# Optimization experiments

Hardware: AMD Instinct MI355X
Metric: run time of the kernel (lower is better)

Reference implementation:

```python
import jax, jax.numpy as jnp
import numpy as np

VOCAB = 50000
WORD_DIM = 300
PAT_LEN = 6
DOC_LEN = 32768


def setup_inputs() -> dict:
    key = jax.random.key(0)
    k1, k2, k3, k4 = jax.random.split(key, 4)
    doc = jax.random.randint(k1, (DOC_LEN,), 0, VOCAB, dtype=jnp.int64)
    embeddings = jax.random.normal(k2, (VOCAB, WORD_DIM), dtype=jnp.float32)
    w = jax.random.normal(k3, (PAT_LEN, PAT_LEN, WORD_DIM), dtype=jnp.float32)
    # original code normalizes each w[i, j] to unit norm at init
    w = w / jnp.linalg.norm(w, axis=-1, keepdims=True)
    b = jax.random.normal(k4, (PAT_LEN, PAT_LEN), dtype=jnp.float32)
    return {"doc": doc, "embeddings": embeddings, "w": w, "b": b}


def reference(doc, embeddings, w, b):
    p = w.shape[0]
    # Only the superdiagonal (i, i+1) of the transition matrix is nonzero.
    idx = jnp.arange(p - 1)
    w_sd = w[idx, idx + 1]          # [p-1, d]
    b_sd = b[idx, idx + 1]          # [p-1]

    x = embeddings[doc]             # [T, d] embedding gather
    # vals[t, i] = sigmoid(w[i,i+1] . x_t + b[i,i+1])   -> [T, p-1]
    vals = jax.nn.sigmoid(x @ w_sd.T + b_sd)

    start = jnp.zeros((p,), dtype=vals.dtype).at[0].set(1.0)

    def step(hidden, v_t):
        # hidden @ T_t: new[j] = hidden[j-1] * vals[t, j-1] for j >= 1
        shifted = hidden[:-1] * v_t                       # [p-1]
        new_hidden = jnp.concatenate([jnp.zeros((1,), hidden.dtype), shifted]) + start
        return new_hidden, new_hidden[-1]                 # score contribution = hidden @ final

    _, contribs = jax.lax.scan(step, start, vals)
    return jnp.sum(contribs)
```

## Files before the change

kernel.cpp:

```cpp
#include <hip/hip_runtime.h>

#define T_LEN 32768
#define DIM   300
#define NCH   75
#define NP    5

__device__ __forceinline__ float fast_sigmoid(float z) {
    return 1.0f / (1.0f + __expf(-z));
}

__global__ __launch_bounds__(256) void vals_kernel(
    const int*   __restrict__ doc,
    const float* __restrict__ emb,
    const float* __restrict__ w,
    const float* __restrict__ b,
    float*       __restrict__ vals)
{
    __shared__ float lds_w[NP][DIM];
    __shared__ float lds_b[NP];

    const int tid = threadIdx.x;

    for (int c = tid; c < NP * NCH; c += 256) {
        const int i  = c / NCH;
        const int cc = c - i * NCH;
        const float4 v = *reinterpret_cast<const float4*>(w + (size_t)(7 * i + 1) * DIM + 4 * cc);
        *reinterpret_cast<float4*>(&lds_w[i][4 * cc]) = v;
    }
    if (tid < NP) lds_b[tid] = b[7 * tid + 1];
    __syncthreads();

    const int g   = tid >> 4;
    const int sub = tid & 15;
    const int t   = blockIdx.x * 16 + g;

    const float* __restrict__ xrow = emb + (size_t)doc[t] * DIM;

    float a0 = 0.f, a1 = 0.f, a2 = 0.f, a3 = 0.f, a4 = 0.f;
    #pragma unroll
    for (int r = 0; r < 5; ++r) {
        const int c = sub + 16 * r;
        if (c < NCH) {
            const float4 xv = *reinterpret_cast<const float4*>(xrow + 4 * c);
            const float4 w0 = *reinterpret_cast<const float4*>(&lds_w[0][4 * c]);
            const float4 w1 = *reinterpret_cast<const float4*>(&lds_w[1][4 * c]);
            const float4 w2 = *reinterpret_cast<const float4*>(&lds_w[2][4 * c]);
            const float4 w3 = *reinterpret_cast<const float4*>(&lds_w[3][4 * c]);
            const float4 w4 = *reinterpret_cast<const float4*>(&lds_w[4][4 * c]);
            a0 += xv.x * w0.x + xv.y * w0.y + xv.z * w0.z + xv.w * w0.w;
            a1 += xv.x * w1.x + xv.y * w1.y + xv.z * w1.z + xv.w * w1.w;
            a2 += xv.x * w2.x + xv.y * w2.y + xv.z * w2.z + xv.w * w2.w;
            a3 += xv.x * w3.x + xv.y * w3.y + xv.z * w3.z + xv.w * w3.w;
            a4 += xv.x * w4.x + xv.y * w4.y + xv.z * w4.z + xv.w * w4.w;
        }
    }

    #pragma unroll
    for (int off = 8; off >= 1; off >>= 1) {
        a0 += __shfl_xor(a0, off);
        a1 += __shfl_xor(a1, off);
        a2 += __shfl_xor(a2, off);
        a3 += __shfl_xor(a3, off);
        a4 += __shfl_xor(a4, off);
    }

    if (sub < NP) {
        const float a = (sub == 0) ? a0 : (sub == 1) ? a1 : (sub == 2) ? a2
                       : (sub == 3) ? a3 : a4;
        vals[sub * T_LEN + t] = fast_sigmoid(a + lds_b[sub]);
    }
}

__global__ __launch_bounds__(256) void reduce_kernel(
    const float* __restrict__ vals,
    float*       __restrict__ out)
{
    const int s = blockIdx.x * 256 + threadIdx.x;
    float p = 0.f;
    if (s <= T_LEN - NP) {
        p = vals[s]
          * vals[1 * T_LEN + s + 1]
          * vals[2 * T_LEN + s + 2]
          * vals[3 * T_LEN + s + 3]
          * vals[4 * T_LEN + s + 4];
    }
    #pragma unroll
    for (int off = 32; off >= 1; off >>= 1) p += __shfl_xor(p, off);

    __shared__ float partial[4];
    if ((threadIdx.x & 63) == 0) partial[threadIdx.x >> 6] = p;
    __syncthreads();
    if (threadIdx.x == 0)
        atomicAdd(out, partial[0] + partial[1] + partial[2] + partial[3]);
}

extern "C" void kernel_launch(void* const* d_in, const int* in_sizes, int n_in,
                              void* d_out, int out_size, void* d_ws, size_t ws_size,
                              hipStream_t stream) {
    const int*   doc = (const int*)  d_in[0];
    const float* emb = (const float*)d_in[1];
    const float* w   = (const float*)d_in[2];
    const float* b   = (const float*)d_in[3];
    float*       out = (float*)d_out;
    float*       vals = (float*)d_ws;

    hipMemsetAsync(out, 0, sizeof(float), stream);

    vals_kernel<<<T_LEN / 16, 256, 0, stream>>>(doc, emb, w, b, vals);
    reduce_kernel<<<(T_LEN + 255) / 256, 256, 0, stream>>>(vals, out);
}
```

Before: 102.6 us.

## Fuse sigmoid-vals and product-reduce kernels with halo rows in LDS

Merges the two kernels into one: each block computes sigmoid values for its 16 tokens plus 4 halo tokens, keeps them in LDS, and forms the diagonal 5-way products and atomic sum locally. This removes the workspace round trip and the second kernel launch. The embedding row loads are issued before the weight staging to overlap gather latency with the LDS fill, and launch bounds request higher occupancy. The cost is recomputing 4 extra rows per block (25% extra gather and dot-product work) and one atomic per block.

```diff
diff --git a/kernel.cpp b/kernel.cpp
--- a/kernel.cpp
+++ b/kernel.cpp
@@ -4,94 +4,131 @@
 #define DIM   300
 #define NCH   75
 #define NP    5
+#define TB    16
+#define ROWS  20
 
 __device__ __forceinline__ float fast_sigmoid(float z) {
     return 1.0f / (1.0f + __expf(-z));
 }
 
-__global__ __launch_bounds__(256) void vals_kernel(
+#define ACC(xv, c)                                                              \
+    {                                                                           \
+        const float4 w0 = *reinterpret_cast<const float4*>(&lds_w[0][4 * (c)]); \
+        const float4 w1 = *reinterpret_cast<const float4*>(&lds_w[1][4 * (c)]); \
+        const float4 w2 = *reinterpret_cast<const float4*>(&lds_w[2][4 * (c)]); \
+        const float4 w3 = *reinterpret_cast<const float4*>(&lds_w[3][4 * (c)]); \
+        const float4 w4 = *reinterpret_cast<const float4*>(&lds_w[4][4 * (c)]); \
+        a0 += (xv).x * w0.x + (xv).y * w0.y + (xv).z * w0.z + (xv).w * w0.w;    \
+        a1 += (xv).x * w1.x + (xv).y * w1.y + (xv).z * w1.z + (xv).w * w1.w;    \
+        a2 += (xv).x * w2.x + (xv).y * w2.y + (xv).z * w2.z + (xv).w * w2.w;    \
+        a3 += (xv).x * w3.x + (xv).y * w3.y + (xv).z * w3.z + (xv).w * w3.w;    \
+        a4 += (xv).x * w4.x + (xv).y * w4.y + (xv).z * w4.z + (xv).w * w4.w;    \
+    }
+
+__global__ __launch_bounds__(256, 8) void fused_kernel(
     const int*   __restrict__ doc,
     const float* __restrict__ emb,
     const float* __restrict__ w,
     const float* __restrict__ b,
-    float*       __restrict__ vals)
+    float*       __restrict__ out)
 {
     __shared__ float lds_w[NP][DIM];
     __shared__ float lds_b[NP];
+    __shared__ float lds_v[ROWS][NP];
 
     const int tid = threadIdx.x;
+    const int g   = tid >> 4;
+    const int sub = tid & 15;
+    const int t0  = blockIdx.x * TB;
+
+    const int  tA = t0 + g;
+    const bool vA = (tA < T_LEN);
+    const float* __restrict__ xrowA = emb + (size_t)(vA ? doc[tA] : 0) * DIM;
+
+    const float4 xa0 = *reinterpret_cast<const float4*>(xrowA + 4 * (sub));
+    const float4 xa1 = *reinterpret_cast<const float4*>(xrowA + 4 * (sub + 16));
+    const float4 xa2 = *reinterpret_cast<const float4*>(xrowA + 4 * (sub + 32));
+    const float4 xa3 = *reinterpret_cast<const float4*>(xrowA + 4 * (sub + 48));
+    float4 xa4 = make_float4(0.f, 0.f, 0.f, 0.f);
+    if (sub < NCH - 64)
+        xa4 = *reinterpret_cast<const float4*>(xrowA + 4 * (sub + 64));
 
     for (int c = tid; c < NP * NCH; c += 256) {
         const int i  = c / NCH;
         const int cc = c - i * NCH;
-        const float4 v = *reinterpret_cast<const float4*>(w + (size_t)(7 * i + 1) * DIM + 4 * cc);
-        *reinterpret_cast<float4*>(&lds_w[i][4 * cc]) = v;
+        *reinterpret_cast<float4*>(&lds_w[i][4 * cc]) =
+            *reinterpret_cast<const float4*>(w + (size_t)(7 * i + 1) * DIM + 4 * cc);
     }
     if (tid < NP) lds_b[tid] = b[7 * tid + 1];
     __syncthreads();
 
-    const int g   = tid >> 4;
-    const int sub = tid & 15;
-    const int t   = blockIdx.x * 16 + g;
-
-    const float* __restrict__ xrow = emb + (size_t)doc[t] * DIM;
-
-    float a0 = 0.f, a1 = 0.f, a2 = 0.f, a3 = 0.f, a4 = 0.f;
-    #pragma unroll
-    for (int r = 0; r < 5; ++r) {
-        const int c = sub + 16 * r;
-        if (c < NCH) {
-            const float4 xv = *reinterpret_cast<const float4*>(xrow + 4 * c);
-            const float4 w0 = *reinterpret_cast<const float4*>(&lds_w[0][4 * c]);
-            const float4 w1 = *reinterpret_cast<const float4*>(&lds_w[1][4 * c]);
-            const float4 w2 = *reinterpret_cast<const float4*>(&lds_w[2][4 * c]);
-            const float4 w3 = *reinterpret_cast<const float4*>(&lds_w[3][4 * c]);
-            const float4 w4 = *reinterpret_cast<const float4*>(&lds_w[4][4 * c]);
-            a0 += xv.x * w0.x + xv.y * w0.y + xv.z * w0.z + xv.w * w0.w;
-            a1 += xv.x * w1.x + xv.y * w1.y + xv.z * w1.z + xv.w * w1.w;
-            a2 += xv.x * w2.x + xv.y * w2.y + xv.z * w2.z + xv.w * w2.w;
-            a3 += xv.x * w3.x + xv.y * w3.y + xv.z * w3.z + xv.w * w3.w;
-            a4 += xv.x * w4.x + xv.y * w4.y + xv.z * w4.z + xv.w * w4.w;
+    {
+        float a0 = 0.f, a1 = 0.f, a2 = 0.f, a3 = 0.f, a4 = 0.f;
+        ACC(xa0, sub);
+        ACC(xa1, sub + 16);
+        ACC(xa2, sub + 32);
+        ACC(xa3, sub + 48);
+        if (sub < NCH - 64) ACC(xa4, sub + 64);
+        #pragma unroll
+        for (int off = 8; off >= 1; off >>= 1) {
+            a0 += __shfl_xor(a0, off);
+            a1 += __shfl_xor(a1, off);
+            a2 += __shfl_xor(a2, off);
+            a3 += __shfl_xor(a3, off);
+            a4 += __shfl_xor(a4, off);
+        }
+        if (sub < NP) {
+            const float a = (sub == 0) ? a0 : (sub == 1) ? a1 : (sub == 2) ? a2
+                           : (sub == 3) ? a3 : a4;
+            lds_v[g][sub] = vA ? fast_sigmoid(a + lds_b[sub]) : 0.f;
         }
     }
 
-    #pragma unroll
-    for (int off = 8; off >= 1; off >>= 1) {
-        a0 += __shfl_xor(a0, off);
-        a1 += __shfl_xor(a1, off);
-        a2 += __shfl_xor(a2, off);
-        a3 += __shfl_xor(a3, off);
-        a4 += __shfl_xor(a4, off);
+    if (g < ROWS - TB) {
+        const int  tB = t0 + TB + g;
+        const bool vB = (tB < T_LEN);
+        const float* __restrict__ xrowB = emb + (size_t)(vB ? doc[tB] : 0) * DIM;
+
+        float a0 = 0.f, a1 = 0.f, a2 = 0.f, a3 = 0.f, a4 = 0.f;
+        const float4 xb0 = *reinterpret_cast<const float4*>(xrowB + 4 * (sub));
+        const float4 xb1 = *reinterpret_cast<const float4*>(xrowB + 4 * (sub + 16));
+        const float4 xb2 = *reinterpret_cast<const float4*>(xrowB + 4 * (sub + 32));
+        const float4 xb3 = *reinterpret_cast<const float4*>(xrowB + 4 * (sub + 48));
+        ACC(xb0, sub);
+        ACC(xb1, sub + 16);
+        ACC(xb2, sub + 32);
+        ACC(xb3, sub + 48);
+        if (sub < NCH - 64) {
+            const float4 xb4 = *reinterpret_cast<const float4*>(xrowB + 4 * (sub + 64));
+            ACC(xb4, sub + 64);
+        }
+        #pragma unroll
+        for (int off = 8; off >= 1; off >>= 1) {
+            a0 += __shfl_xor(a0, off);
+            a1 += __shfl_xor(a1, off);
+            a2 += __shfl_xor(a2, off);
+            a3 += __shfl_xor(a3, off);
+            a4 += __shfl_xor(a4, off);
+        }
+        if (sub < NP) {
+            const float a = (sub == 0) ? a0 : (sub == 1) ? a1 : (sub == 2) ? a2
+                           : (sub == 3) ? a3 : a4;
+            lds_v[TB + g][sub] = vB ? fast_sigmoid(a + lds_b[sub]) : 0.f;
+        }
     }
+    __syncthreads();
 
-    if (sub < NP) {
-        const float a = (sub == 0) ? a0 : (sub == 1) ? a1 : (sub == 2) ? a2
-                       : (sub == 3) ? a3 : a4;
-        vals[sub * T_LEN + t] = fast_sigmoid(a + lds_b[sub]);
+    if (tid < 64) {
+        float p = 0.f;
+        const int s = t0 + tid;
+        if (tid < TB && s <= T_LEN - NP) {
+            p = lds_v[tid + 0][0] * lds_v[tid + 1][1] * lds_v[tid + 2][2]
+              * lds_v[tid + 3][3] * lds_v[tid + 4][4];
+        }
+        #pragma unroll
+        for (int off = 32; off >= 1; off >>= 1) p += __shfl_xor(p, off);
+        if (tid == 0) atomicAdd(out, p);
     }
-}
-
-__global__ __launch_bounds__(256) void reduce_kernel(
-    const float* __restrict__ vals,
-    float*       __restrict__ out)
-{
-    const int s = blockIdx.x * 256 + threadIdx.x;
-    float p = 0.f;
-    if (s <= T_LEN - NP) {
-        p = vals[s]
-          * vals[1 * T_LEN + s + 1]
-          * vals[2 * T_LEN + s + 2]
-          * vals[3 * T_LEN + s + 3]
-          * vals[4 * T_LEN + s + 4];
-    }
-    #pragma unroll
-    for (int off = 32; off >= 1; off >>= 1) p += __shfl_xor(p, off);
-
-    __shared__ float partial[4];
-    if ((threadIdx.x & 63) == 0) partial[threadIdx.x >> 6] = p;
-    __syncthreads();
-    if (threadIdx.x == 0)
-        atomicAdd(out, partial[0] + partial[1] + partial[2] + partial[3]);
 }
 
 extern "C" void kernel_launch(void* const* d_in, const int* in_sizes, int n_in,
@@ -102,10 +139,7 @@
     const float* w   = (const float*)d_in[2];
     const float* b   = (const float*)d_in[3];
     float*       out = (float*)d_out;
-    float*       vals = (float*)d_ws;
 
     hipMemsetAsync(out, 0, sizeof(float), stream);
-
-    vals_kernel<<<T_LEN / 16, 256, 0, stream>>>(doc, emb, w, b, vals);
-    reduce_kernel<<<(T_LEN + 255) / 256, 256, 0, stream>>>(vals, out);
+    fused_kernel<<<T_LEN / TB, 256, 0, stream>>>(doc, emb, w, b, out);
 }
```

After: 160.9 us. 1.57x slower.
